# Kernel tuning notes

Hardware: AMD Instinct MI355X
Metric: run time of the kernel (lower is better)

The kernel has to match this reference:

```python
import jax, jax.numpy as jnp
import numpy as np

B, T, N, P, L = 8, 96, 20000, 12, 3
D = 32          # d_model (forced by channel-count identity d_model+96 == 4*d_model)
C = 4 * D       # 128 channels inside the linearized conv layers
M = 64          # random_feature_dim
TAU = 0.25
EPS = 1e-6      # numerical_stabilizer in random_feature_map


def _proj_matrix(m, d, seed=0):
    # create_random_matrix: stacked transposed-Q blocks from QR of gaussian blocks,
    # scaled row-wise by norms of a gaussian matrix (scaling=0).
    rng = np.random.RandomState(seed)
    blocks = []
    n_full = m // d
    for _ in range(n_full):
        q, _ = np.linalg.qr(rng.randn(d, d))
        blocks.append(q.T)
    rem = m - n_full * d
    if rem:
        q, _ = np.linalg.qr(rng.randn(d, d))
        blocks.append(q.T[:rem])
    mat = np.vstack(blocks)
    mult = np.linalg.norm(rng.randn(m, d), axis=1)
    return jnp.asarray(mult[:, None] * mat, dtype=jnp.float32)


def setup_inputs() -> dict:
    key = jax.random.key(0)
    ks = jax.random.split(key, 12)
    g = lambda k, shape, s=0.05: jax.random.normal(k, shape, jnp.float32) * s
    return {
        "x": jax.random.normal(ks[0], (B, T, N), jnp.float32),
        "x_mark": jax.random.uniform(ks[1], (B, T, 2), dtype=jnp.float32),
        "node_emb": g(ks[2], (N, D), 0.1),
        "time_tab": g(ks[3], (T, D), 0.1),
        "week_tab": g(ks[4], (7, D), 0.1),
        "input_w": g(ks[5], (D, 3 * T)),
        "input_b": jnp.zeros((D,), jnp.float32),
        "w1_w": g(ks[6], (D, 3 * D)),
        "w1_b": jnp.zeros((D,), jnp.float32),
        "w2_w": g(ks[7], (D, 3 * D)),
        "w2_b": jnp.zeros((D,), jnp.float32),
        "in_w": g(ks[8], (L, C, C)),
        "in_b": jnp.zeros((L, C), jnp.float32),
        "out_w": g(ks[9], (L, C, C)),
        "out_b": jnp.zeros((L, C), jnp.float32),
        "ln_g": jnp.ones((L, C), jnp.float32),
        "ln_b": jnp.zeros((L, C), jnp.float32),
        "reg_w": g(ks[10], (P, 2 * C)),
        "reg_b": jnp.zeros((P,), jnp.float32),
        "proj": _proj_matrix(M, D, seed=0),
    }


def _rfm(data, proj, is_query):
    # FAVOR+ positive random features (head dim == 1 folded out; shapes are [B,N,d])
    d = data.shape[-1]
    data = data * (float(d) ** -0.25)            # h(x) normalizer d^{-1/4}
    ratio = 1.0 / np.sqrt(float(proj.shape[0]))
    dash = jnp.einsum('bnd,md->bnm', data, proj)
    diag = 0.5 * jnp.sum(data * data, axis=-1, keepdims=True)
    if is_query:
        stab = jnp.max(dash, axis=-1, keepdims=True)          # per-row max
    else:
        stab = jnp.max(dash, axis=(1, 2), keepdims=True)      # max over features AND nodes
    return ratio * (jnp.exp(dash - diag - stab) + EPS)


def _linear_kernel(v, phi_q, phi_k):
    # associativity trick: (phi_q (phi_k^T v)) / (phi_q (phi_k^T 1))
    kv = jnp.einsum('bnm,bnc->bmc', phi_k, v)
    num = jnp.einsum('bnm,bmc->bnc', phi_q, kv)
    den = jnp.einsum('bnm,bm->bn', phi_q, jnp.sum(phi_k, axis=1))
    return num / den[..., None]


def reference(x, x_mark, node_emb, time_tab, week_tab, input_w, input_b,
              w1_w, w1_b, w2_w, w2_b, in_w, in_b, out_w, out_b,
              ln_g, ln_b, reg_w, reg_b, proj):
    Bq, Tq, Nq = x.shape
    marks = jax.lax.stop_gradient(x_mark)
    tod_idx = jnp.clip((marks[:, -1, 0] * Tq).astype(jnp.int32), 0, Tq - 1)
    dow_idx = jnp.clip((marks[:, -1, 1] * 7.0).astype(jnp.int32), 0, 6)
    time_e = jnp.broadcast_to(time_tab[tod_idx][:, None, :], (Bq, Nq, D))
    week_e = jnp.broadcast_to(week_tab[dow_idx][:, None, :], (Bq, Nq, D))
    node_e = jnp.broadcast_to(node_emb[None], (Bq, Nq, D))

    # input embedding over the flattened (feature-major) [3*T] channel axis
    tod_f = jnp.broadcast_to(x_mark[:, :, 0:1], (Bq, Tq, Nq))
    dow_f = jnp.broadcast_to(x_mark[:, :, 1:2], (Bq, Tq, Nq))
    feat = jnp.concatenate([x, tod_f, dow_f], axis=1)          # (B, 3T, N)
    x_in = jnp.einsum('bkn,ck->bnc', feat, input_w) + input_b  # (B, N, D)

    xg = jnp.concatenate([node_e, time_e, week_e], axis=-1)        # (B,N,3D)
    h = jnp.concatenate([x_in, node_e, time_e, week_e], axis=-1)   # (B,N,4D)

    inv_sqrt_tau = 1.0 / np.sqrt(TAU)
    nv1 = (jnp.einsum('bng,cg->bnc', xg, w1_w) + w1_b) * inv_sqrt_tau
    nv2 = (jnp.einsum('bng,cg->bnc', xg, w2_w) + w2_b) * inv_sqrt_tau
    # same node vectors (hence same data-derived seed / projection) every layer
    phi_q = _rfm(nv1, proj, True)    # (B,N,M)
    phi_k = _rfm(nv2, proj, False)   # (B,N,M)

    skip = h
    for i in range(L):
        res = h
        u = jax.nn.sigmoid(h @ in_w[i].T + in_b[i]) * (h @ out_w[i].T + out_b[i])
        u = _linear_kernel(u, phi_q, phi_k)
        h = u + res
        mu = jnp.mean(h, axis=-1, keepdims=True)
        var = jnp.var(h, axis=-1, keepdims=True)
        h = (h - mu) * jax.lax.rsqrt(var + 1e-5) * ln_g[i] + ln_b[i]

    out = jnp.concatenate([skip, h], axis=-1) @ reg_w.T + reg_b  # (B,N,P)
    return jnp.swapaxes(out, 1, 2)                               # (B,P,N)
```

## Files before the change

kernel.cpp:

```cpp
#include <hip/hip_runtime.h>

typedef unsigned short u16;
typedef __attribute__((ext_vector_type(8))) __bf16 bf16x8;
typedef __attribute__((ext_vector_type(4))) float f32x4;

#define BB 8
#define TT 96
#define NN 20000
#define NP 20160
#define PP 12
#define LL 3
#define DD 32
#define CC 128
#define MM 64
#define NB3 105
#define NB5 313
#define NB1 313

constexpr float KSC  = 0.8408964152537145f;
constexpr float KSC2 = 0.7071067811865476f;

__device__ inline u16 f2bf(float f){
  unsigned u = __float_as_uint(f);
  u = (u + 0x7fffu + ((u >> 16) & 1u)) >> 16;
  return (u16)u;
}
__device__ inline float bf2f(u16 h){ return __uint_as_float(((unsigned)h) << 16); }
__device__ inline unsigned fmapu(float f){
  unsigned u = __float_as_uint(f);
  return (u & 0x80000000u) ? ~u : (u | 0x80000000u);
}
__device__ inline float funmap(unsigned u){
  return (u & 0x80000000u) ? __uint_as_float(u & 0x7fffffffu) : __uint_as_float(~u);
}
__device__ inline unsigned pk2(float a, float b){
  return (unsigned)f2bf(a) | ((unsigned)f2bf(b) << 16);
}

__global__ void k0_prep(const float* xm, const float* time_tab, const float* week_tab,
                        const float* w1w, const float* w1b, const float* w2w, const float* w2b,
                        const float* inw, const float* inb, const float* proj,
                        float* bv1, float* bv2, float* sbd1, float* sbd2,
                        float* bc1, float* bc2, float* mb, int* tod, int* dow,
                        unsigned* cmx, float* ksum, float* qmat, float* emat)
{
  __shared__ float sT[BB][DD], sWk[BB][DD];
  __shared__ float sB1[BB][DD], sB2[BB][DD];
  __shared__ float sW1G[DD][DD], sW2G[DD][DD], sPJ[MM][DD];
  __shared__ int sTod[BB], sDow[BB];
  int tid = threadIdx.x;
  ksum[tid] = 0.f;
  for (int i = tid; i < DD*DD; i += 512){
    int c = i >> 5, g = i & 31;
    sW1G[c][g] = w1w[c*96 + g];
    sW2G[c][g] = w2w[c*96 + g];
  }
  for (int i = tid; i < MM*DD; i += 512) sPJ[i >> 5][i & 31] = proj[i];
  if (tid < BB){
    float t0 = xm[(tid*TT + TT-1)*2 + 0];
    float t1 = xm[(tid*TT + TT-1)*2 + 1];
    int ti = (int)(t0 * (float)TT); ti = min(max(ti, 0), TT-1);
    int di = (int)(t1 * 7.0f);      di = min(max(di, 0), 6);
    sTod[tid] = ti; sDow[tid] = di; tod[tid] = ti; dow[tid] = di;
  }
  if (tid < MM) cmx[tid] = fmapu(-3e38f);
  __syncthreads();
  if (tid < BB*DD){
    int b = tid >> 5, g = tid & 31;
    sT[b][g]  = time_tab[sTod[b]*DD + g];
    sWk[b][g] = week_tab[sDow[b]*DD + g];
  }
  __syncthreads();
  {
    int which = tid >> 8, b = (tid >> 5) & 7, c = tid & 31;
    const float* w  = which ? w2w : w1w;
    const float* wb = which ? w2b : w1b;
    float s = wb[c];
    for (int g = 0; g < DD; g++)
      s += sT[b][g]*w[c*96 + 32 + g] + sWk[b][g]*w[c*96 + 64 + g];
    if (which){ bv2[b*DD+c] = s; sB2[b][c] = s; }
    else      { bv1[b*DD+c] = s; sB1[b][c] = s; }
  }
  __syncthreads();
  for (int e = tid; e < 2*DD*MM; e += 512){
    int set = e >> 11, g = (e >> 6) & 31, m = e & 63;
    float s = 0.f;
    if (set == 0){ for (int c = 0; c < DD; c++) s += sW1G[c][g]*sPJ[m][c]; }
    else         { for (int c = 0; c < DD; c++) s += sW2G[c][g]*sPJ[m][c]; }
    qmat[e] = KSC * s;
  }
  {
    int set = tid >> 8, g = (tid >> 3) & 31, b = tid & 7;
    float s = 0.f;
    if (set == 0){ for (int c = 0; c < DD; c++) s += sW1G[c][g]*sB1[b][c]; }
    else         { for (int c = 0; c < DD; c++) s += sW2G[c][g]*sB2[b][c]; }
    emat[tid] = KSC2 * s;
  }
  {
    int b = tid >> 6, m = tid & 63;
    float s1 = 0.f, s2 = 0.f;
    for (int c = 0; c < DD; c++){
      float p = sPJ[m][c];
      s1 += sB1[b][c]*p; s2 += sB2[b][c]*p;
    }
    sbd1[b*MM+m] = KSC * s1;
    sbd2[b*MM+m] = KSC * s2;
  }
  if (tid < 16){
    int b = tid & 7;
    float s = 0.f;
    if (tid >> 3){ for (int c = 0; c < DD; c++) s += sB2[b][c]*sB2[b][c]; bc2[b] = 0.5f*KSC2*s; }
    else         { for (int c = 0; c < DD; c++) s += sB1[b][c]*sB1[b][c]; bc1[b] = 0.5f*KSC2*s; }
  }
  if (tid < 256){
    int b = tid >> 5, c = tid & 31;
    float s = inb[c];
    for (int t = 0; t < TT; t++){
      float m0 = xm[(b*TT+t)*2+0], m1 = xm[(b*TT+t)*2+1];
      s += m0 * inw[c*288 + 96 + t] + m1 * inw[c*288 + 192 + t];
    }
    mb[b*DD+c] = s;
  }
}

__global__ __launch_bounds__(256) void k1_node(
    const float* node_emb, const float* w1w, const float* w2w,
    const float* qmat, const float* emat,
    const float* gin_w, const float* gout_w,
    float* sd1, float* sd2, float* sq1, float* sq2,
    float* cr1, float* cr2, unsigned* cmx,
    u16* wbf, float* kvz)
{
  __shared__ float sQ1[DD*MM], sQ2[DD*MM];
  __shared__ float sW1[DD*DD], sW2[DD*DD];
  __shared__ float sE[2*DD*BB];
  __shared__ unsigned sCM[MM];
  int tid = threadIdx.x;
  int gid = blockIdx.x*256 + tid;
  const int TOT = NB1*256;
  for (int i = gid; i < LL*BB*MM*CC; i += TOT) kvz[i] = 0.f;
  for (int i = gid; i < 2*LL*CC*CC; i += TOT){
    int which = i / (LL*CC*CC);
    int r = i - which*(LL*CC*CC);
    wbf[i] = f2bf((which ? gout_w : gin_w)[r]);
  }
  for (int i = tid; i < DD*MM; i += 256){ sQ1[i] = qmat[i]; sQ2[i] = qmat[DD*MM + i]; }
  for (int i = tid; i < DD*DD; i += 256){
    sW1[i] = w1w[(i>>5)*96 + (i&31)];
    sW2[i] = w2w[(i>>5)*96 + (i&31)];
  }
  for (int i = tid; i < 2*DD*BB; i += 256) sE[i] = emat[i];
  if (tid < MM) sCM[tid] = fmapu(-3e38f);
  __syncthreads();
  int r = tid >> 2, q = tid & 3;
  int n = blockIdx.x*64 + r;
  bool valid = n < NN;
  int nc = valid ? n : 0;
  float nd[DD];
  #pragma unroll
  for (int g = 0; g < DD; g += 4){
    float4 v = *(const float4*)&node_emb[nc*DD + g];
    nd[g] = v.x; nd[g+1] = v.y; nd[g+2] = v.z; nd[g+3] = v.w;
  }
  float s1v[16], s2v[16];
  #pragma unroll
  for (int j = 0; j < 16; j++){ s1v[j] = 0.f; s2v[j] = 0.f; }
  #pragma unroll
  for (int g = 0; g < DD; g++){
    float xg = nd[g];
    #pragma unroll
    for (int jj = 0; jj < 16; jj += 4){
      float4 a1 = *(const float4*)&sQ1[g*MM + q*16 + jj];
      float4 a2 = *(const float4*)&sQ2[g*MM + q*16 + jj];
      s1v[jj+0] += xg*a1.x; s1v[jj+1] += xg*a1.y; s1v[jj+2] += xg*a1.z; s1v[jj+3] += xg*a1.w;
      s2v[jj+0] += xg*a2.x; s2v[jj+1] += xg*a2.y; s2v[jj+2] += xg*a2.z; s2v[jj+3] += xg*a2.w;
    }
  }
  if (valid){
    #pragma unroll
    for (int jj = 0; jj < 16; jj += 4){
      *(float4*)&sd1[(size_t)n*MM + q*16 + jj] = make_float4(s1v[jj], s1v[jj+1], s1v[jj+2], s1v[jj+3]);
      *(float4*)&sd2[(size_t)n*MM + q*16 + jj] = make_float4(s2v[jj], s2v[jj+1], s2v[jj+2], s2v[jj+3]);
    }
    #pragma unroll
    for (int j = 0; j < 16; j++)
      atomicMax(&sCM[q*16 + j], fmapu(s2v[j]));
  }
  float sqp1 = 0.f, sqp2 = 0.f;
  #pragma unroll
  for (int c8 = 0; c8 < 8; c8++){
    int c = q*8 + c8;
    float d1 = 0.f, d2 = 0.f;
    #pragma unroll
    for (int g = 0; g < DD; g += 4){
      float4 w1v = *(const float4*)&sW1[c*DD + g];
      float4 w2v = *(const float4*)&sW2[c*DD + g];
      d1 += nd[g]*w1v.x + nd[g+1]*w1v.y + nd[g+2]*w1v.z + nd[g+3]*w1v.w;
      d2 += nd[g]*w2v.x + nd[g+1]*w2v.y + nd[g+2]*w2v.z + nd[g+3]*w2v.w;
    }
    sqp1 += d1*d1; sqp2 += d2*d2;
  }
  sqp1 += __shfl_xor(sqp1, 1); sqp1 += __shfl_xor(sqp1, 2);
  sqp2 += __shfl_xor(sqp2, 1); sqp2 += __shfl_xor(sqp2, 2);
  if (q == 0 && valid){
    sq1[n] = 0.5f*KSC2*sqp1;
    sq2[n] = 0.5f*KSC2*sqp2;
  }
  {
    float cA1 = 0.f, cB1 = 0.f, cA2 = 0.f, cB2 = 0.f;
    #pragma unroll
    for (int g = 0; g < DD; g++){
      float xg = nd[g];
      cA1 += xg*sE[g*8 + 2*q];
      cB1 += xg*sE[g*8 + 2*q + 1];
      cA2 += xg*sE[256 + g*8 + 2*q];
      cB2 += xg*sE[256 + g*8 + 2*q + 1];
    }
    if (valid){
      cr1[(2*q)*NN + n]     = cA1;
      cr1[(2*q+1)*NN + n]   = cB1;
      cr2[(2*q)*NN + n]     = cA2;
      cr2[(2*q+1)*NN + n]   = cB2;
    }
  }
  __syncthreads();
  if (tid < MM) atomicMax(&cmx[tid], sCM[tid]);
}

__global__ void k0b_stab(const unsigned* cmx, const float* sbd2, float* stab){
  int lane = threadIdx.x;
  float cm = funmap(cmx[lane]);
  for (int b = 0; b < BB; b++){
    float v = cm + sbd2[b*MM + lane];
    #pragma unroll
    for (int off = 32; off; off >>= 1) v = fmaxf(v, __shfl_xor(v, off));
    if (lane == 0) stab[b] = v;
  }
}

__global__ __launch_bounds__(256) void k1b_phi(
    const float* sd1, const float* sd2, const float* sq1, const float* sq2,
    const float* cr1, const float* cr2, const float* sbd1, const float* sbd2,
    const float* bc1, const float* bc2, const float* stab,
    u16* phiq, u16* phikt, float* ksum)
{
  __shared__ u16 sT[MM][264];
  __shared__ float sQb[MM], sKb[MM];
  __shared__ float sRed[256];
  int tid = threadIdx.x;
  int b = blockIdx.y, n0 = blockIdx.x*256;
  if (tid < MM){
    sQb[tid] = sbd1[b*MM + tid];
    sKb[tid] = sbd2[b*MM + tid] - bc2[b] - stab[b];
  }
  __syncthreads();
  int n = n0 + tid;
  bool v = n < NN;
  int nc = v ? n : 0;
  float dq[MM];
  const float* s1r = sd1 + (size_t)nc*MM;
  #pragma unroll
  for (int m = 0; m < MM; m += 4){
    float4 t = *(const float4*)&s1r[m];
    dq[m]=t.x; dq[m+1]=t.y; dq[m+2]=t.z; dq[m+3]=t.w;
  }
  float rm = -3e38f;
  #pragma unroll
  for (int m = 0; m < MM; m++) rm = fmaxf(rm, dq[m] + sQb[m]);
  float diagq = sq1[nc] + cr1[b*NN + nc] + bc1[b];
  u16* pqr = phiq + ((size_t)(b*NN) + nc)*MM;
  #pragma unroll
  for (int m = 0; m < MM; m += 8){
    float p[8];
    #pragma unroll
    for (int j = 0; j < 8; j++){
      float ev = dq[m+j] + sQb[m+j] - rm - diagq;
      p[j] = 0.125f*__expf(ev) + 1.25e-7f;
    }
    uint4 w = { pk2(p[0],p[1]), pk2(p[2],p[3]), pk2(p[4],p[5]), pk2(p[6],p[7]) };
    if (v) *(uint4*)&pqr[m] = w;
  }
  const float* s2r = sd2 + (size_t)nc*MM;
  float diagk = sq2[nc] + cr2[b*NN + nc];
  #pragma unroll
  for (int m = 0; m < MM; m++){
    float ev = s2r[m] + sKb[m] - diagk;
    float pv = v ? (0.125f*__expf(ev) + 1.25e-7f) : 0.f;
    sT[m][tid] = f2bf(pv);
  }
  __syncthreads();
  {
    int m = tid >> 2, q = tid & 3;
    float s = 0.f;
    for (int j = 0; j < 64; j++) s += bf2f(sT[m][q*64 + j]);
    sRed[tid] = s;
  }
  __syncthreads();
  if (tid < MM){
    float s = sRed[tid*4] + sRed[tid*4+1] + sRed[tid*4+2] + sRed[tid*4+3];
    atomicAdd(&ksum[b*MM + tid], s);
  }
  {
    int m = tid >> 2, q = tid & 3;
    int nb = n0 + q*64;
    if (nb + 64 <= NP){
      u16* dst = phikt + (size_t)(b*MM + m)*NP + nb;
      #pragma unroll
      for (int j = 0; j < 64; j += 8)
        *(uint4*)&dst[j] = *(const uint4*)&sT[m][q*64 + j];
    }
  }
}

__global__ __launch_bounds__(256) void k2_embed(
    const float* x, const float* node_emb, const float* time_tab, const float* week_tab,
    const float* inw, const float* mb, const int* tod, const int* dow,
    u16* skip)
{
  __shared__ float sWt[TT*DD];
  __shared__ float sMB[DD], sTE[DD], sWE[DD];
  int tid = threadIdx.x;
  int b = blockIdx.y;
  for (int i = tid; i < TT*DD; i += 256){
    int t = i >> 5, c = i & 31;
    sWt[i] = inw[c*288 + t];
  }
  if (tid < DD){
    sMB[tid] = mb[b*DD + tid];
    sTE[tid] = time_tab[tod[b]*DD + tid];
    sWE[tid] = week_tab[dow[b]*DD + tid];
  }
  __syncthreads();
  int n = blockIdx.x*256 + tid;
  bool valid = n < NN;
  int nc = valid ? n : 0;
  float acc[DD];
  #pragma unroll
  for (int c = 0; c < DD; c++) acc[c] = sMB[c];
  const float* xb = x + (size_t)b*TT*NN + nc;
  for (int t = 0; t < TT; t++){
    float xv = xb[(size_t)t*NN];
    #pragma unroll
    for (int c = 0; c < DD; c++) acc[c] += xv * sWt[t*DD + c];
  }
  if (!valid) return;
  float nodev[DD];
  #pragma unroll
  for (int g = 0; g < DD; g += 4){
    float4 v = *(const float4*)&node_emb[n*DD + g];
    nodev[g] = v.x; nodev[g+1] = v.y; nodev[g+2] = v.z; nodev[g+3] = v.w;
  }
  auto chv = [&](int c)->float{
    if (c < 32)  return acc[c];
    if (c < 64)  return nodev[c-32];
    if (c < 96)  return sTE[c-64];
    return sWE[c-96];
  };
  u16* dst = skip + (size_t)(b*NN + n)*CC;
  #pragma unroll
  for (int g = 0; g < CC; g += 8){
    uint4 w;
    w.x = pk2(chv(g+0), chv(g+1));
    w.y = pk2(chv(g+2), chv(g+3));
    w.z = pk2(chv(g+4), chv(g+5));
    w.w = pk2(chv(g+6), chv(g+7));
    *(uint4*)&dst[g] = w;
  }
}

__global__ __launch_bounds__(256,2) void k3_gate(
    const u16* hin, const u16* wbf, const float* inb, const float* outb,
    const u16* phikt, float* kv, int layer)
{
  __shared__ u16 sUT[4][32*72];
  int tid = threadIdx.x;
  int b = blockIdx.y, blk = blockIdx.x;
  int lane = tid & 63, wave = tid >> 6, quad = lane >> 4, l15 = lane & 15;
  u16* myUT = &sUT[wave][0];

  float bi[2], bo[2];
  #pragma unroll
  for (int nt = 0; nt < 2; nt++){
    int co = wave*32 + nt*16 + l15;
    bi[nt] = inb[layer*CC + co];
    bo[nt] = outb[layer*CC + co];
  }
  bf16x8 bw[4][4];
  #pragma unroll
  for (int nt = 0; nt < 4; nt++){
    int which = nt >> 1;
    int co = wave*32 + (nt & 1)*16 + l15;
    const u16* wp = wbf + ((size_t)(which*LL + layer)*CC + co)*CC;
    #pragma unroll
    for (int ks = 0; ks < 4; ks++)
      bw[ks][nt] = *(const bf16x8*)&wp[ks*32 + quad*8];
  }
  f32x4 kvacc[4][2] = {};
  const u16* hbase = hin + (size_t)(b*NN)*CC;

  for (int ch = 0; ch < 3; ch++){
    int n0 = blk*192 + ch*64;
    f32x4 acc[4][4] = {};
    bf16x8 af[2][4];
    #pragma unroll
    for (int mt = 0; mt < 4; mt++)
      af[0][mt] = *(const bf16x8*)&hbase[(size_t)(n0 + mt*16 + l15)*CC + quad*8];
    #pragma unroll
    for (int ks = 0; ks < 4; ks++){
      int cur = ks & 1, nxt = cur ^ 1;
      if (ks < 3){
        #pragma unroll
        for (int mt = 0; mt < 4; mt++)
          af[nxt][mt] = *(const bf16x8*)&hbase[(size_t)(n0 + mt*16 + l15)*CC + (ks+1)*32 + quad*8];
      }
      #pragma unroll
      for (int mt = 0; mt < 4; mt++)
        #pragma unroll
        for (int nt = 0; nt < 4; nt++)
          acc[mt][nt] = __builtin_amdgcn_mfma_f32_16x16x32_bf16(af[cur][mt], bw[ks][nt], acc[mt][nt], 0, 0, 0);
    }
    #pragma unroll
    for (int mt = 0; mt < 4; mt++){
      int r0 = mt*16 + quad*4;
      #pragma unroll
      for (int nt = 0; nt < 2; nt++){
        int cop = nt*16 + l15;
        float uv[4];
        #pragma unroll
        for (int e = 0; e < 4; e++){
          float up = acc[mt][nt][e] + bi[nt];
          float vp = acc[mt][nt+2][e] + bo[nt];
          float u = vp / (1.f + __expf(-up));
          if (n0 + r0 + e >= NN) u = 0.f;
          uv[e] = u;
        }
        ushort4 hv4;
        hv4.x = f2bf(uv[0]); hv4.y = f2bf(uv[1]); hv4.z = f2bf(uv[2]); hv4.w = f2bf(uv[3]);
        *(ushort4*)&myUT[cop*72 + r0] = hv4;
      }
    }
    #pragma unroll
    for (int ks2 = 0; ks2 < 2; ks2++){
      bf16x8 ap[4], bu[2];
      #pragma unroll
      for (int mtp = 0; mtp < 4; mtp++)
        ap[mtp] = *(const bf16x8*)&phikt[(size_t)(b*MM + mtp*16 + l15)*NP + n0 + ks2*32 + quad*8];
      #pragma unroll
      for (int nt2 = 0; nt2 < 2; nt2++)
        bu[nt2] = *(const bf16x8*)&myUT[(nt2*16 + l15)*72 + ks2*32 + quad*8];
      #pragma unroll
      for (int mtp = 0; mtp < 4; mtp++)
        #pragma unroll
        for (int nt2 = 0; nt2 < 2; nt2++)
          kvacc[mtp][nt2] = __builtin_amdgcn_mfma_f32_16x16x32_bf16(ap[mtp], bu[nt2], kvacc[mtp][nt2], 0, 0, 0);
    }
  }
  float* kvb = kv + (size_t)(layer*BB + b)*MM*CC;
  #pragma unroll
  for (int mt = 0; mt < 4; mt++)
    #pragma unroll
    for (int nt2 = 0; nt2 < 2; nt2++)
      #pragma unroll
      for (int e = 0; e < 4; e++)
        atomicAdd(&kvb[(mt*16 + quad*4 + e)*CC + wave*32 + nt2*16 + l15], kvacc[mt][nt2][e]);
}

__global__ void k4_reduce(const float* kv, const float* ksum, u16* kvt, int layer){
  int b = blockIdx.x;
  int tid = threadIdx.x;
  const float* kvb = kv + (size_t)(layer*BB + b)*MM*CC;
  for (int idx = tid; idx < 144*MM; idx += 256){
    int c = idx >> 6, m = idx & 63;
    float v = (c < CC) ? kvb[m*CC + c] : ((c == CC) ? ksum[b*MM + m] : 0.f);
    kvt[(size_t)b*144*MM + idx] = f2bf(v);
  }
}

__global__ __launch_bounds__(256) void k5_attn(
    const u16* hin, u16* hout, const u16* phiq, const u16* kvt,
    const float* lng, const float* lnb, int layer)
{
  __shared__ u16 sH[64*132];
  int tid = threadIdx.x;
  int b = blockIdx.y, n0 = blockIdx.x*64;
  int lane = tid & 63, wave = tid >> 6, quad = lane >> 4, l15 = lane & 15;
  const u16* kvb = kvt + (size_t)b*144*MM;
  {
    int r = wave*16 + (lane >> 2), seg = lane & 3;
    int n = n0 + r;
    const u16* src = hin + (size_t)(b*NN + min(n, NN-1))*CC + seg*32;
    #pragma unroll
    for (int k = 0; k < 32; k += 8){
      uint4 d = *(const uint4*)&src[k];
      *(uint2*)&sH[r*132 + seg*32 + k]     = make_uint2(d.x, d.y);
      *(uint2*)&sH[r*132 + seg*32 + k + 4] = make_uint2(d.z, d.w);
    }
  }
  bf16x8 aq[2];
  #pragma unroll
  for (int ks = 0; ks < 2; ks++)
    aq[ks] = *(const bf16x8*)&phiq[((size_t)(b*NN) + n0 + wave*16 + l15)*MM + ks*32 + quad*8];
  f32x4 nacc[9] = {};
  #pragma unroll
  for (int ks = 0; ks < 2; ks++)
    #pragma unroll
    for (int nt = 0; nt < 9; nt++){
      bf16x8 bk = *(const bf16x8*)&kvb[(nt*16 + l15)*MM + ks*32 + quad*8];
      nacc[nt] = __builtin_amdgcn_mfma_f32_16x16x32_bf16(aq[ks], bk, nacc[nt], 0, 0, 0);
    }
  float lg[8], lb[8];
  #pragma unroll
  for (int nt = 0; nt < 8; nt++){
    lg[nt] = lng[layer*CC + nt*16 + l15];
    lb[nt] = lnb[layer*CC + nt*16 + l15];
  }
  #pragma unroll
  for (int e = 0; e < 4; e++){
    float den = __shfl(nacc[8][e], lane & 48);
    int rml = wave*16 + quad*4 + e;
    float y[8];
    float s1 = 0.f, s2 = 0.f;
    #pragma unroll
    for (int nt = 0; nt < 8; nt++){
      float res = bf2f(sH[rml*132 + nt*16 + l15]);
      float yv = nacc[nt][e]/den + res;
      y[nt] = yv; s1 += yv; s2 += yv*yv;
    }
    #pragma unroll
    for (int off = 1; off < 16; off <<= 1){
      s1 += __shfl_xor(s1, off);
      s2 += __shfl_xor(s2, off);
    }
    float mu = s1 * (1.f/CC);
    float rs = rsqrtf(s2 * (1.f/CC) - mu*mu + 1e-5f);
    #pragma unroll
    for (int nt = 0; nt < 8; nt++){
      int c = nt*16 + l15;
      sH[rml*132 + c] = f2bf((y[nt] - mu)*rs*lg[nt] + lb[nt]);
    }
  }
  {
    int r = wave*16 + (lane >> 2), seg = lane & 3;
    int n = n0 + r;
    if (n < NN){
      u16* dst = hout + (size_t)(b*NN + n)*CC + seg*32;
      #pragma unroll
      for (int k = 0; k < 32; k += 8){
        uint2 a = *(const uint2*)&sH[r*132 + seg*32 + k];
        uint2 c2 = *(const uint2*)&sH[r*132 + seg*32 + k + 4];
        uint4 w = { a.x, a.y, c2.x, c2.y };
        *(uint4*)&dst[k] = w;
      }
    }
  }
}

__global__ __launch_bounds__(256) void k6_final(
    const u16* skip, const u16* hbuf, const float* regw, const float* regb,
    float* out)
{
  __shared__ float sRW[PP*256];
  __shared__ float sRB[PP];
  int tid = threadIdx.x;
  for (int i = tid; i < PP*256; i += 256) sRW[i] = regw[i];
  if (tid < PP) sRB[tid] = regb[tid];
  __syncthreads();
  int b = blockIdx.y;
  int n = blockIdx.x*256 + tid;
  if (n >= NN) return;
  float acc[PP];
  #pragma unroll
  for (int p = 0; p < PP; p++) acc[p] = sRB[p];
  const u16* sr = skip + (size_t)(b*NN + n)*CC;
  const u16* hr = hbuf + (size_t)(b*NN + n)*CC;
  for (int half = 0; half < 2; half++){
    const u16* src = half ? hr : sr;
    int coff = half*128;
    for (int k = 0; k < CC; k += 8){
      uint4 d = *(const uint4*)&src[k];
      float v0 = __uint_as_float(d.x<<16), v1 = __uint_as_float(d.x & 0xffff0000u);
      float v2 = __uint_as_float(d.y<<16), v3 = __uint_as_float(d.y & 0xffff0000u);
      float v4 = __uint_as_float(d.z<<16), v5 = __uint_as_float(d.z & 0xffff0000u);
      float v6 = __uint_as_float(d.w<<16), v7 = __uint_as_float(d.w & 0xffff0000u);
      #pragma unroll
      for (int p = 0; p < PP; p++){
        const float* wr = &sRW[p*256 + coff + k];
        acc[p] += v0*wr[0] + v1*wr[1] + v2*wr[2] + v3*wr[3]
                + v4*wr[4] + v5*wr[5] + v6*wr[6] + v7*wr[7];
      }
    }
  }
  #pragma unroll
  for (int p = 0; p < PP; p++)
    out[(size_t)(b*PP + p)*NN + n] = acc[p];
}

extern "C" void kernel_launch(void* const* d_in, const int* in_sizes, int n_in,
                              void* d_out, int out_size, void* d_ws, size_t ws_size,
                              hipStream_t stream)
{
  const float* x        = (const float*)d_in[0];
  const float* xm       = (const float*)d_in[1];
  const float* node_emb = (const float*)d_in[2];
  const float* time_tab = (const float*)d_in[3];
  const float* week_tab = (const float*)d_in[4];
  const float* input_w  = (const float*)d_in[5];
  const float* input_b  = (const float*)d_in[6];
  const float* w1w      = (const float*)d_in[7];
  const float* w1b      = (const float*)d_in[8];
  const float* w2w      = (const float*)d_in[9];
  const float* w2b      = (const float*)d_in[10];
  const float* inw      = (const float*)d_in[11];
  const float* inb      = (const float*)d_in[12];
  const float* outw     = (const float*)d_in[13];
  const float* outb     = (const float*)d_in[14];
  const float* lng      = (const float*)d_in[15];
  const float* lnb      = (const float*)d_in[16];
  const float* regw     = (const float*)d_in[17];
  const float* regb     = (const float*)d_in[18];
  const float* proj     = (const float*)d_in[19];
  float* out = (float*)d_out;

  char* wsb = (char*)d_ws;
  size_t off = 0;
  auto alloc = [&](size_t bytes)->char*{
    char* p = wsb + off; off += (bytes + 255) & ~(size_t)255; return p;
  };
  u16*   skip  = (u16*)  alloc((size_t)BB*NN*CC*2);
  u16*   hbuf  = (u16*)  alloc((size_t)BB*NN*CC*2);
  u16*   phiq  = (u16*)  alloc((size_t)BB*NN*MM*2);
  u16*   phikt = (u16*)  alloc((size_t)BB*MM*NP*2 + 4096);
  float* sd1   = (float*)alloc((size_t)NN*MM*4);
  float* sd2   = (float*)alloc((size_t)NN*MM*4);
  float* sq1   = (float*)alloc((size_t)NN*4);
  float* sq2   = (float*)alloc((size_t)NN*4);
  float* cr1   = (float*)alloc((size_t)BB*NN*4);
  float* cr2   = (float*)alloc((size_t)BB*NN*4);
  u16*   wbf   = (u16*)  alloc((size_t)2*LL*CC*CC*2);
  float* kv    = (float*)alloc((size_t)LL*BB*MM*CC*4);
  u16*   kvt   = (u16*)  alloc((size_t)BB*144*MM*2);
  float* ksum  = (float*)alloc(BB*MM*4);
  float* bv1   = (float*)alloc(BB*DD*4);
  float* bv2   = (float*)alloc(BB*DD*4);
  float* sbd1  = (float*)alloc(BB*MM*4);
  float* sbd2  = (float*)alloc(BB*MM*4);
  float* bc1   = (float*)alloc(BB*4);
  float* bc2   = (float*)alloc(BB*4);
  float* mb    = (float*)alloc(BB*DD*4);
  int*   tod   = (int*)  alloc(BB*4);
  int*   dow   = (int*)  alloc(BB*4);
  unsigned* cmx= (unsigned*)alloc(MM*4);
  float* stab  = (float*)alloc(BB*4);
  float* qmat  = (float*)alloc(2*DD*MM*4);
  float* emat  = (float*)alloc(2*DD*BB*4);
  (void)ws_size; (void)in_sizes; (void)n_in; (void)out_size;

  k0_prep<<<1, 512, 0, stream>>>(xm, time_tab, week_tab, w1w, w1b, w2w, w2b,
                                 input_w, input_b, proj,
                                 bv1, bv2, sbd1, sbd2, bc1, bc2, mb, tod, dow, cmx, ksum,
                                 qmat, emat);
  k1_node<<<NB1, 256, 0, stream>>>(node_emb, w1w, w2w, qmat, emat, inw, outw,
                                   sd1, sd2, sq1, sq2, cr1, cr2, cmx, wbf, kv);
  k0b_stab<<<1, 64, 0, stream>>>(cmx, sbd2, stab);
  k1b_phi<<<dim3(79, 8), 256, 0, stream>>>(sd1, sd2, sq1, sq2, cr1, cr2,
                                           sbd1, sbd2, bc1, bc2, stab,
                                           phiq, phikt, ksum);
  k2_embed<<<dim3(79, 8), 256, 0, stream>>>(x, node_emb, time_tab, week_tab,
                                            input_w, mb, tod, dow, skip);
  for (int l = 0; l < LL; l++){
    const u16* hi = (l == 0) ? skip : hbuf;
    k3_gate<<<dim3(NB3, 8), 256, 0, stream>>>(hi, wbf, inb, outb, phikt, kv, l);
    k4_reduce<<<8, 256, 0, stream>>>(kv, ksum, kvt, l);
    k5_attn<<<dim3(NB5, 8), 256, 0, stream>>>(hi, hbuf, phiq, kvt, lng, lnb, l);
  }
  k6_final<<<dim3(79, 8), 256, 0, stream>>>(skip, hbuf, regw, regb, out);
}
```

Before: 661.9 us.

## Replace KV atomics with per-block partials, smaller tiles and more blocks

The gate kernel now processes 128 nodes per block instead of 192, with 157 blocks per batch, and targets 3 blocks per SM. It recomputes the u/v projections one output-channel half at a time and streams weights from global memory instead of holding them all in registers. Each block writes its KV partial to its own slice, and a wider reduce kernel sums the partials, which removes the float atomics and the per-layer zeroing. In exchange it reloads the activation tiles twice per chunk and adds partial-buffer traffic of about 157×8×32 KB per layer.

Result: slower. 709.2 us (+7.1%).

```diff
diff --git a/kernel.cpp b/kernel.cpp
--- a/kernel.cpp
+++ b/kernel.cpp
@@ -13,7 +13,7 @@
 #define DD 32
 #define CC 128
 #define MM 64
-#define NB3 105
+#define NB3 157
 #define NB5 313
 #define NB1 313
 
@@ -129,7 +129,7 @@
     const float* gin_w, const float* gout_w,
     float* sd1, float* sd2, float* sq1, float* sq2,
     float* cr1, float* cr2, unsigned* cmx,
-    u16* wbf, float* kvz)
+    u16* wbf)
 {
   __shared__ float sQ1[DD*MM], sQ2[DD*MM];
   __shared__ float sW1[DD*DD], sW2[DD*DD];
@@ -138,7 +138,6 @@
   int tid = threadIdx.x;
   int gid = blockIdx.x*256 + tid;
   const int TOT = NB1*256;
-  for (int i = gid; i < LL*BB*MM*CC; i += TOT) kvz[i] = 0.f;
   for (int i = gid; i < 2*LL*CC*CC; i += TOT){
     int which = i / (LL*CC*CC);
     int r = i - which*(LL*CC*CC);
@@ -368,9 +367,9 @@
   }
 }
 
-__global__ __launch_bounds__(256,2) void k3_gate(
+__global__ __launch_bounds__(256,3) void k3_gate(
     const u16* hin, const u16* wbf, const float* inb, const float* outb,
-    const u16* phikt, float* kv, int layer)
+    const u16* phikt, float* kvp, int layer)
 {
   __shared__ u16 sUT[4][32*72];
   int tid = threadIdx.x;
@@ -380,99 +379,91 @@
 
   float bi[2], bo[2];
   #pragma unroll
-  for (int nt = 0; nt < 2; nt++){
-    int co = wave*32 + nt*16 + l15;
-    bi[nt] = inb[layer*CC + co];
-    bo[nt] = outb[layer*CC + co];
-  }
-  bf16x8 bw[4][4];
-  #pragma unroll
-  for (int nt = 0; nt < 4; nt++){
-    int which = nt >> 1;
-    int co = wave*32 + (nt & 1)*16 + l15;
-    const u16* wp = wbf + ((size_t)(which*LL + layer)*CC + co)*CC;
-    #pragma unroll
-    for (int ks = 0; ks < 4; ks++)
-      bw[ks][nt] = *(const bf16x8*)&wp[ks*32 + quad*8];
-  }
+  for (int p = 0; p < 2; p++){
+    int co = wave*32 + p*16 + l15;
+    bi[p] = inb[layer*CC + co];
+    bo[p] = outb[layer*CC + co];
+  }
+  const u16* wub = wbf + ((size_t)(0*LL + layer)*CC)*CC;
+  const u16* wvb = wbf + ((size_t)(1*LL + layer)*CC)*CC;
+  const u16* hbase = hin + (size_t)(b*NN)*CC;
   f32x4 kvacc[4][2] = {};
-  const u16* hbase = hin + (size_t)(b*NN)*CC;
-
-  for (int ch = 0; ch < 3; ch++){
-    int n0 = blk*192 + ch*64;
-    f32x4 acc[4][4] = {};
-    bf16x8 af[2][4];
-    #pragma unroll
-    for (int mt = 0; mt < 4; mt++)
-      af[0][mt] = *(const bf16x8*)&hbase[(size_t)(n0 + mt*16 + l15)*CC + quad*8];
-    #pragma unroll
-    for (int ks = 0; ks < 4; ks++){
-      int cur = ks & 1, nxt = cur ^ 1;
-      if (ks < 3){
+
+  for (int ch = 0; ch < 2; ch++){
+    int n0 = blk*128 + ch*64;
+    #pragma unroll
+    for (int p = 0; p < 2; p++){
+      int co = wave*32 + p*16 + l15;
+      f32x4 accu[4] = {}, accv[4] = {};
+      #pragma unroll
+      for (int ks = 0; ks < 4; ks++){
+        bf16x8 bu = *(const bf16x8*)&wub[(size_t)co*CC + ks*32 + quad*8];
+        bf16x8 bv = *(const bf16x8*)&wvb[(size_t)co*CC + ks*32 + quad*8];
         #pragma unroll
-        for (int mt = 0; mt < 4; mt++)
-          af[nxt][mt] = *(const bf16x8*)&hbase[(size_t)(n0 + mt*16 + l15)*CC + (ks+1)*32 + quad*8];
+        for (int mt = 0; mt < 4; mt++){
+          bf16x8 a = *(const bf16x8*)&hbase[(size_t)(n0 + mt*16 + l15)*CC + ks*32 + quad*8];
+          accu[mt] = __builtin_amdgcn_mfma_f32_16x16x32_bf16(a, bu, accu[mt], 0, 0, 0);
+          accv[mt] = __builtin_amdgcn_mfma_f32_16x16x32_bf16(a, bv, accv[mt], 0, 0, 0);
+        }
       }
       #pragma unroll
-      for (int mt = 0; mt < 4; mt++)
-        #pragma unroll
-        for (int nt = 0; nt < 4; nt++)
-          acc[mt][nt] = __builtin_amdgcn_mfma_f32_16x16x32_bf16(af[cur][mt], bw[ks][nt], acc[mt][nt], 0, 0, 0);
-    }
-    #pragma unroll
-    for (int mt = 0; mt < 4; mt++){
-      int r0 = mt*16 + quad*4;
-      #pragma unroll
-      for (int nt = 0; nt < 2; nt++){
-        int cop = nt*16 + l15;
+      for (int mt = 0; mt < 4; mt++){
+        int r0 = mt*16 + quad*4;
         float uv[4];
         #pragma unroll
         for (int e = 0; e < 4; e++){
-          float up = acc[mt][nt][e] + bi[nt];
-          float vp = acc[mt][nt+2][e] + bo[nt];
+          float up = accu[mt][e] + bi[p];
+          float vp = accv[mt][e] + bo[p];
           float u = vp / (1.f + __expf(-up));
           if (n0 + r0 + e >= NN) u = 0.f;
           uv[e] = u;
         }
         ushort4 hv4;
         hv4.x = f2bf(uv[0]); hv4.y = f2bf(uv[1]); hv4.z = f2bf(uv[2]); hv4.w = f2bf(uv[3]);
-        *(ushort4*)&myUT[cop*72 + r0] = hv4;
+        *(ushort4*)&myUT[(p*16 + l15)*72 + r0] = hv4;
       }
     }
     #pragma unroll
     for (int ks2 = 0; ks2 < 2; ks2++){
-      bf16x8 ap[4], bu[2];
+      bf16x8 ap[4], bu2[2];
       #pragma unroll
       for (int mtp = 0; mtp < 4; mtp++)
         ap[mtp] = *(const bf16x8*)&phikt[(size_t)(b*MM + mtp*16 + l15)*NP + n0 + ks2*32 + quad*8];
       #pragma unroll
       for (int nt2 = 0; nt2 < 2; nt2++)
-        bu[nt2] = *(const bf16x8*)&myUT[(nt2*16 + l15)*72 + ks2*32 + quad*8];
+        bu2[nt2] = *(const bf16x8*)&myUT[(nt2*16 + l15)*72 + ks2*32 + quad*8];
       #pragma unroll
       for (int mtp = 0; mtp < 4; mtp++)
         #pragma unroll
         for (int nt2 = 0; nt2 < 2; nt2++)
-          kvacc[mtp][nt2] = __builtin_amdgcn_mfma_f32_16x16x32_bf16(ap[mtp], bu[nt2], kvacc[mtp][nt2], 0, 0, 0);
-    }
-  }
-  float* kvb = kv + (size_t)(layer*BB + b)*MM*CC;
+          kvacc[mtp][nt2] = __builtin_amdgcn_mfma_f32_16x16x32_bf16(ap[mtp], bu2[nt2], kvacc[mtp][nt2], 0, 0, 0);
+    }
+  }
+  float* myp = kvp + ((size_t)blk*BB + b)*(MM*CC);
   #pragma unroll
   for (int mt = 0; mt < 4; mt++)
     #pragma unroll
     for (int nt2 = 0; nt2 < 2; nt2++)
       #pragma unroll
-      for (int e = 0; e < 4; e++)
-        atomicAdd(&kvb[(mt*16 + quad*4 + e)*CC + wave*32 + nt2*16 + l15], kvacc[mt][nt2][e]);
-}
-
-__global__ void k4_reduce(const float* kv, const float* ksum, u16* kvt, int layer){
-  int b = blockIdx.x;
-  int tid = threadIdx.x;
-  const float* kvb = kv + (size_t)(layer*BB + b)*MM*CC;
-  for (int idx = tid; idx < 144*MM; idx += 256){
-    int c = idx >> 6, m = idx & 63;
-    float v = (c < CC) ? kvb[m*CC + c] : ((c == CC) ? ksum[b*MM + m] : 0.f);
-    kvt[(size_t)b*144*MM + idx] = f2bf(v);
+      for (int e = 0; e < 4; e++){
+        int m = mt*16 + quad*4 + e;
+        int c = wave*32 + nt2*16 + l15;
+        myp[m*CC + c] = kvacc[mt][nt2][e];
+      }
+}
+
+__global__ __launch_bounds__(256) void k4_reduce(const float* kvp, const float* ksum, u16* kvt){
+  int b = blockIdx.y;
+  int idx = blockIdx.x*256 + threadIdx.x;
+  float s = 0.f;
+  for (int blk = 0; blk < NB3; blk++)
+    s += kvp[((size_t)blk*BB + b)*(MM*CC) + idx];
+  int m = idx >> 7, c = idx & 127;
+  kvt[(size_t)b*144*MM + c*MM + m] = f2bf(s);
+  if (idx < MM) kvt[(size_t)b*144*MM + 128*MM + idx] = f2bf(ksum[b*MM + idx]);
+  if (idx >= 8192 - 15*MM){
+    int j = idx - (8192 - 15*MM);
+    kvt[(size_t)b*144*MM + 129*MM + j] = 0;
   }
 }
 
@@ -637,7 +628,7 @@
   float* cr1   = (float*)alloc((size_t)BB*NN*4);
   float* cr2   = (float*)alloc((size_t)BB*NN*4);
   u16*   wbf   = (u16*)  alloc((size_t)2*LL*CC*CC*2);
-  float* kv    = (float*)alloc((size_t)LL*BB*MM*CC*4);
+  float* kvp   = (float*)alloc((size_t)NB3*BB*MM*CC*4);
   u16*   kvt   = (u16*)  alloc((size_t)BB*144*MM*2);
   float* ksum  = (float*)alloc(BB*MM*4);
   float* bv1   = (float*)alloc(BB*DD*4);
@@ -660,7 +651,7 @@
                                  bv1, bv2, sbd1, sbd2, bc1, bc2, mb, tod, dow, cmx, ksum,
                                  qmat, emat);
   k1_node<<<NB1, 256, 0, stream>>>(node_emb, w1w, w2w, qmat, emat, inw, outw,
-                                   sd1, sd2, sq1, sq2, cr1, cr2, cmx, wbf, kv);
+                                   sd1, sd2, sq1, sq2, cr1, cr2, cmx, wbf);
   k0b_stab<<<1, 64, 0, stream>>>(cmx, sbd2, stab);
   k1b_phi<<<dim3(79, 8), 256, 0, stream>>>(sd1, sd2, sq1, sq2, cr1, cr2,
                                            sbd1, sbd2, bc1, bc2, stab,
@@ -669,8 +660,8 @@
                                             input_w, mb, tod, dow, skip);
   for (int l = 0; l < LL; l++){
     const u16* hi = (l == 0) ? skip : hbuf;
-    k3_gate<<<dim3(NB3, 8), 256, 0, stream>>>(hi, wbf, inb, outb, phikt, kv, l);
-    k4_reduce<<<8, 256, 0, stream>>>(kv, ksum, kvt, l);
+    k3_gate<<<dim3(NB3, 8), 256, 0, stream>>>(hi, wbf, inb, outb, phikt, kvp, l);
+    k4_reduce<<<dim3(32, 8), 256, 0, stream>>>(kvp, ksum, kvt);
     k5_attn<<<dim3(NB5, 8), 256, 0, stream>>>(hi, hbuf, phiq, kvt, lng, lnb, l);
   }
   k6_final<<<dim3(79, 8), 256, 0, stream>>>(skip, hbuf, regw, regb, out);
```

## Fuse attention-apply/layernorm of layer l with gating/KV accumulation of layer l+1

Applied to the files above, without the earlier changes.

Adds a k53 kernel that applies the linear-attention output, residual and layernorm for one layer, writes h, then reuses the normalized tile from LDS to compute the next layer's gated projection and accumulate phi_k^T u into kv. The per-layer sequence k3/k4/k5 becomes k3, then two fused k53 launches, then a final k5. This drops one global read of h per layer boundary and two kernel launches. Supporting changes widen NP so phikt stores need no bounds check, and remove the manual double-buffered A-fragment prefetch in k3. The in-place hin==hout use relies on each block reading only its own rows before writing them.

After: 702.9 us. 6.2% more time.

```diff
diff --git a/kernel.cpp b/kernel.cpp
--- a/kernel.cpp
+++ b/kernel.cpp
@@ -7,7 +7,7 @@
 #define BB 8
 #define TT 96
 #define NN 20000
-#define NP 20160
+#define NP 20224
 #define PP 12
 #define LL 3
 #define DD 32
@@ -303,12 +303,10 @@
   {
     int m = tid >> 2, q = tid & 3;
     int nb = n0 + q*64;
-    if (nb + 64 <= NP){
-      u16* dst = phikt + (size_t)(b*MM + m)*NP + nb;
-      #pragma unroll
-      for (int j = 0; j < 64; j += 8)
-        *(uint4*)&dst[j] = *(const uint4*)&sT[m][q*64 + j];
-    }
+    u16* dst = phikt + (size_t)(b*MM + m)*NP + nb;
+    #pragma unroll
+    for (int j = 0; j < 64; j += 8)
+      *(uint4*)&dst[j] = *(const uint4*)&sT[m][q*64 + j];
   }
 }
 
@@ -401,23 +399,17 @@
   for (int ch = 0; ch < 3; ch++){
     int n0 = blk*192 + ch*64;
     f32x4 acc[4][4] = {};
-    bf16x8 af[2][4];
-    #pragma unroll
-    for (int mt = 0; mt < 4; mt++)
-      af[0][mt] = *(const bf16x8*)&hbase[(size_t)(n0 + mt*16 + l15)*CC + quad*8];
     #pragma unroll
     for (int ks = 0; ks < 4; ks++){
-      int cur = ks & 1, nxt = cur ^ 1;
-      if (ks < 3){
-        #pragma unroll
-        for (int mt = 0; mt < 4; mt++)
-          af[nxt][mt] = *(const bf16x8*)&hbase[(size_t)(n0 + mt*16 + l15)*CC + (ks+1)*32 + quad*8];
-      }
+      bf16x8 a[4];
+      #pragma unroll
+      for (int mt = 0; mt < 4; mt++)
+        a[mt] = *(const bf16x8*)&hbase[(size_t)(n0 + mt*16 + l15)*CC + ks*32 + quad*8];
       #pragma unroll
       for (int mt = 0; mt < 4; mt++)
         #pragma unroll
         for (int nt = 0; nt < 4; nt++)
-          acc[mt][nt] = __builtin_amdgcn_mfma_f32_16x16x32_bf16(af[cur][mt], bw[ks][nt], acc[mt][nt], 0, 0, 0);
+          acc[mt][nt] = __builtin_amdgcn_mfma_f32_16x16x32_bf16(a[mt], bw[ks][nt], acc[mt][nt], 0, 0, 0);
     }
     #pragma unroll
     for (int mt = 0; mt < 4; mt++){
@@ -474,6 +466,170 @@
     float v = (c < CC) ? kvb[m*CC + c] : ((c == CC) ? ksum[b*MM + m] : 0.f);
     kvt[(size_t)b*144*MM + idx] = f2bf(v);
   }
+}
+
+__global__ __launch_bounds__(256,2) void k53(
+    const u16* hin, u16* hout, const u16* phiq, const u16* kvt,
+    const float* lng, const float* lnb,
+    const u16* wbf, const float* g_inb, const float* g_outb, const u16* phikt,
+    float* kv, int lat, int lgt)
+{
+  __shared__ u16 sH[64*136];
+  __shared__ u16 sUT[4][32*72];
+  int tid = threadIdx.x;
+  int b = blockIdx.y, blk = blockIdx.x;
+  int lane = tid & 63, wave = tid >> 6, quad = lane >> 4, l15 = lane & 15;
+  u16* myUT = &sUT[wave][0];
+  const u16* kvb = kvt + (size_t)b*144*MM;
+  float lg[8], lb[8];
+  #pragma unroll
+  for (int nt = 0; nt < 8; nt++){
+    lg[nt] = lng[lat*CC + nt*16 + l15];
+    lb[nt] = lnb[lat*CC + nt*16 + l15];
+  }
+  float bi[2], bo[2];
+  #pragma unroll
+  for (int p = 0; p < 2; p++){
+    int co = wave*32 + p*16 + l15;
+    bi[p] = g_inb[lgt*CC + co];
+    bo[p] = g_outb[lgt*CC + co];
+  }
+  bf16x8 bw[4][4];
+  #pragma unroll
+  for (int nt = 0; nt < 4; nt++){
+    int which = nt >> 1;
+    int co = wave*32 + (nt & 1)*16 + l15;
+    const u16* wp = wbf + ((size_t)(which*LL + lgt)*CC + co)*CC;
+    #pragma unroll
+    for (int ks = 0; ks < 4; ks++)
+      bw[ks][nt] = *(const bf16x8*)&wp[ks*32 + quad*8];
+  }
+  f32x4 kvacc[4][2] = {};
+  const u16* hb_in = hin + (size_t)(b*NN)*CC;
+  u16* hb_out = hout + (size_t)(b*NN)*CC;
+
+  for (int ch = 0; ch < 3; ch++){
+    int n0 = blk*192 + ch*64;
+    {
+      int r = wave*16 + (lane >> 2), seg = lane & 3;
+      int n = n0 + r;
+      const u16* src = hb_in + (size_t)min(n, NN-1)*CC + seg*32;
+      #pragma unroll
+      for (int k = 0; k < 32; k += 8){
+        uint4 d = *(const uint4*)&src[k];
+        *(uint2*)&sH[r*136 + seg*32 + k]     = make_uint2(d.x, d.y);
+        *(uint2*)&sH[r*136 + seg*32 + k + 4] = make_uint2(d.z, d.w);
+      }
+    }
+    bf16x8 aq[2];
+    #pragma unroll
+    for (int ks = 0; ks < 2; ks++)
+      aq[ks] = *(const bf16x8*)&phiq[((size_t)(b*NN) + n0 + wave*16 + l15)*MM + ks*32 + quad*8];
+    f32x4 nacc[9] = {};
+    #pragma unroll
+    for (int ks = 0; ks < 2; ks++)
+      #pragma unroll
+      for (int nt = 0; nt < 9; nt++){
+        bf16x8 bk = *(const bf16x8*)&kvb[(nt*16 + l15)*MM + ks*32 + quad*8];
+        nacc[nt] = __builtin_amdgcn_mfma_f32_16x16x32_bf16(aq[ks], bk, nacc[nt], 0, 0, 0);
+      }
+    #pragma unroll
+    for (int e = 0; e < 4; e++){
+      float den = __shfl(nacc[8][e], lane & 48);
+      int rml = wave*16 + quad*4 + e;
+      float y[8];
+      float s1 = 0.f, s2 = 0.f;
+      #pragma unroll
+      for (int nt = 0; nt < 8; nt++){
+        float res = bf2f(sH[rml*136 + nt*16 + l15]);
+        float yv = nacc[nt][e]/den + res;
+        y[nt] = yv; s1 += yv; s2 += yv*yv;
+      }
+      #pragma unroll
+      for (int off = 1; off < 16; off <<= 1){
+        s1 += __shfl_xor(s1, off);
+        s2 += __shfl_xor(s2, off);
+      }
+      float mu = s1 * (1.f/CC);
+      float rs = rsqrtf(s2 * (1.f/CC) - mu*mu + 1e-5f);
+      #pragma unroll
+      for (int nt = 0; nt < 8; nt++){
+        int c = nt*16 + l15;
+        sH[rml*136 + c] = f2bf((y[nt] - mu)*rs*lg[nt] + lb[nt]);
+      }
+    }
+    {
+      int r = wave*16 + (lane >> 2), seg = lane & 3;
+      int n = n0 + r;
+      if (n < NN){
+        u16* dst = hb_out + (size_t)n*CC + seg*32;
+        #pragma unroll
+        for (int k = 0; k < 32; k += 8){
+          uint2 a = *(const uint2*)&sH[r*136 + seg*32 + k];
+          uint2 c2 = *(const uint2*)&sH[r*136 + seg*32 + k + 4];
+          uint4 w = { a.x, a.y, c2.x, c2.y };
+          *(uint4*)&dst[k] = w;
+        }
+      }
+    }
+    __syncthreads();
+    f32x4 accm[4][4] = {};
+    #pragma unroll
+    for (int ks = 0; ks < 4; ks++){
+      bf16x8 a[4];
+      #pragma unroll
+      for (int mt = 0; mt < 4; mt++)
+        a[mt] = *(const bf16x8*)&sH[(mt*16 + l15)*136 + ks*32 + quad*8];
+      #pragma unroll
+      for (int mt = 0; mt < 4; mt++)
+        #pragma unroll
+        for (int nt = 0; nt < 4; nt++)
+          accm[mt][nt] = __builtin_amdgcn_mfma_f32_16x16x32_bf16(a[mt], bw[ks][nt], accm[mt][nt], 0, 0, 0);
+    }
+    #pragma unroll
+    for (int mt = 0; mt < 4; mt++){
+      int r0 = mt*16 + quad*4;
+      #pragma unroll
+      for (int nt = 0; nt < 2; nt++){
+        float uv[4];
+        #pragma unroll
+        for (int e = 0; e < 4; e++){
+          float up = accm[mt][nt][e] + bi[nt];
+          float vp = accm[mt][nt+2][e] + bo[nt];
+          float u = vp / (1.f + __expf(-up));
+          if (n0 + r0 + e >= NN) u = 0.f;
+          uv[e] = u;
+        }
+        ushort4 hv4;
+        hv4.x = f2bf(uv[0]); hv4.y = f2bf(uv[1]); hv4.z = f2bf(uv[2]); hv4.w = f2bf(uv[3]);
+        *(ushort4*)&myUT[(nt*16 + l15)*72 + r0] = hv4;
+      }
+    }
+    #pragma unroll
+    for (int ks2 = 0; ks2 < 2; ks2++){
+      bf16x8 ap[4], bu2[2];
+      #pragma unroll
+      for (int mtp = 0; mtp < 4; mtp++)
+        ap[mtp] = *(const bf16x8*)&phikt[(size_t)(b*MM + mtp*16 + l15)*NP + n0 + ks2*32 + quad*8];
+      #pragma unroll
+      for (int nt2 = 0; nt2 < 2; nt2++)
+        bu2[nt2] = *(const bf16x8*)&myUT[(nt2*16 + l15)*72 + ks2*32 + quad*8];
+      #pragma unroll
+      for (int mtp = 0; mtp < 4; mtp++)
+        #pragma unroll
+        for (int nt2 = 0; nt2 < 2; nt2++)
+          kvacc[mtp][nt2] = __builtin_amdgcn_mfma_f32_16x16x32_bf16(ap[mtp], bu2[nt2], kvacc[mtp][nt2], 0, 0, 0);
+    }
+    __syncthreads();
+  }
+  float* kvw = kv + (size_t)(lgt*BB + b)*MM*CC;
+  #pragma unroll
+  for (int mt = 0; mt < 4; mt++)
+    #pragma unroll
+    for (int nt2 = 0; nt2 < 2; nt2++)
+      #pragma unroll
+      for (int e = 0; e < 4; e++)
+        atomicAdd(&kvw[(mt*16 + quad*4 + e)*CC + wave*32 + nt2*16 + l15], kvacc[mt][nt2][e]);
 }
 
 __global__ __launch_bounds__(256) void k5_attn(
@@ -667,11 +823,14 @@
                                            phiq, phikt, ksum);
   k2_embed<<<dim3(79, 8), 256, 0, stream>>>(x, node_emb, time_tab, week_tab,
                                             input_w, mb, tod, dow, skip);
-  for (int l = 0; l < LL; l++){
-    const u16* hi = (l == 0) ? skip : hbuf;
-    k3_gate<<<dim3(NB3, 8), 256, 0, stream>>>(hi, wbf, inb, outb, phikt, kv, l);
-    k4_reduce<<<8, 256, 0, stream>>>(kv, ksum, kvt, l);
-    k5_attn<<<dim3(NB5, 8), 256, 0, stream>>>(hi, hbuf, phiq, kvt, lng, lnb, l);
-  }
+  k3_gate<<<dim3(NB3, 8), 256, 0, stream>>>(skip, wbf, inb, outb, phikt, kv, 0);
+  k4_reduce<<<8, 256, 0, stream>>>(kv, ksum, kvt, 0);
+  k53<<<dim3(NB3, 8), 256, 0, stream>>>(skip, hbuf, phiq, kvt, lng, lnb,
+                                        wbf, inb, outb, phikt, kv, 0, 1);
+  k4_reduce<<<8, 256, 0, stream>>>(kv, ksum, kvt, 1);
+  k53<<<dim3(NB3, 8), 256, 0, stream>>>(hbuf, hbuf, phiq, kvt, lng, lnb,
+                                        wbf, inb, outb, phikt, kv, 1, 2);
+  k4_reduce<<<8, 256, 0, stream>>>(kv, ksum, kvt, 2);
+  k5_attn<<<dim3(NB5, 8), 256, 0, stream>>>(hbuf, hbuf, phiq, kvt, lng, lnb, 2);
   k6_final<<<dim3(79, 8), 256, 0, stream>>>(skip, hbuf, regw, regb, out);
 }
```
